# Kernel optimization log

Hardware: AMD Instinct MI355X
Metric: run time of the kernel (lower is better)

## Reference

```python
import jax, jax.numpy as jnp
import numpy as np

N_NODES = 8192
N_EDGES = 262144  # avg degree 32
F_IN = 128
F_OUT = 128


def setup_inputs() -> dict:
    key = jax.random.key(0)
    k1, k2, k3, k4 = jax.random.split(key, 4)
    x = jax.random.normal(k1, (N_NODES, F_IN), dtype=jnp.float32)
    edge_index = jax.random.randint(k2, (2, N_EDGES), 0, N_NODES, dtype=jnp.int32)
    # xavier_uniform-scale random W; B is a learned param (zeros at init, but
    # use random values so the x@B^T branch is exercised numerically)
    scale = np.float32(1.0 / np.sqrt(F_IN))
    W = jax.random.normal(k3, (F_OUT, F_IN), dtype=jnp.float32) * scale
    B = jax.random.normal(k4, (F_OUT, F_IN), dtype=jnp.float32) * scale
    return {"x": x, "edge_index": edge_index, "W": W, "B": B}


def reference(x, edge_index, W, B):
    num_nodes = x.shape[0]
    src, dst = edge_index[0], edge_index[1]
    # Dense adjacency: A[i, j] = 1 iff edge j -> i (duplicate edges collapse to 1,
    # matching torch's adj[dst, src] = 1.0 assignment semantics)
    A = jnp.zeros((num_nodes, num_nodes), dtype=jnp.float32).at[dst, src].set(1.0)
    # In-degree (counts duplicate edges, matching torch.bincount); degree-0 -> 1
    deg = jax.ops.segment_sum(jnp.ones_like(dst, dtype=jnp.float32), dst,
                              num_segments=num_nodes)
    deg = jnp.where(deg == 0, 1.0, deg)
    # D_inv @ A @ x @ W^T + x @ B^T; D_inv is diagonal -> row-scale by 1/deg
    msg = A @ (x @ W.T)           # [N, F_OUT]
    out = msg / deg[:, None] + x @ B.T
    return out
```

## Files before the change

### kernel.cpp

```cpp
#include <hip/hip_runtime.h>
#include <hip/hip_bf16.h>

constexpr int NN = 8192;
constexpr int NE = 262144;
constexpr int FD = 128;
constexpr int CAP = 64;

constexpr size_t H_OFF     = 0;
constexpr size_t H_BYTES   = (size_t)NN * FD * 2;
constexpr size_t CNT_OFF   = H_OFF + H_BYTES;
constexpr size_t CNT_BYTES = (size_t)NN * 4;
constexpr size_t COL_OFF   = CNT_OFF + CNT_BYTES;
constexpr size_t COL_BYTES = (size_t)NN * CAP * 4;
constexpr size_t UB_OFF    = COL_OFF + COL_BYTES;

constexpr int FILL_BLOCKS = 512;
constexpr int GEMM_BLOCKS = 512;

typedef __attribute__((ext_vector_type(8))) short short8;
typedef __attribute__((ext_vector_type(4))) float f32x4;

__device__ __forceinline__ short f2b(float f) {
  union { __hip_bfloat16 b; short s; } u;
  u.b = __float2bfloat16(f);
  return u.s;
}

__device__ __forceinline__ short8 cvt8(float4 a, float4 b) {
  return short8{f2b(a.x), f2b(a.y), f2b(a.z), f2b(a.w),
                f2b(b.x), f2b(b.y), f2b(b.z), f2b(b.w)};
}

__global__ __launch_bounds__(256) void prep_kernel(
    const float* __restrict__ W, const float* __restrict__ Bm,
    short* __restrict__ ub, unsigned int* __restrict__ cnt) {
  const int t = blockIdx.x * 256 + threadIdx.x;
  const float4 f = (t < 4096) ? ((const float4*)W)[t] : ((const float4*)Bm)[t - 4096];
  ((short4*)ub)[t] = short4{f2b(f.x), f2b(f.y), f2b(f.z), f2b(f.w)};
  if (t < 2048) ((uint4*)cnt)[t] = uint4{0u, 0u, 0u, 0u};
}

__global__ __launch_bounds__(256) void fillgemm_kernel(
    const int* __restrict__ ei, unsigned int* __restrict__ cnt,
    int* __restrict__ col, const float* __restrict__ x,
    const short* __restrict__ ub, __hip_bfloat16* __restrict__ h,
    float* __restrict__ out) {
  const int tid = threadIdx.x;

  if (blockIdx.x < FILL_BLOCKS) {
    const int e = (blockIdx.x * 256 + tid) * 2;
    const int2 s2 = *(const int2*)(ei + e);
    const int2 d2 = *(const int2*)(ei + NE + e);
#pragma unroll
    for (int r = 0; r < 2; ++r) {
      const int src = (&s2.x)[r];
      const int dst = (&d2.x)[r];
      const unsigned int pos = atomicAdd(&cnt[dst], 1u);
      if (pos < CAP) col[(size_t)dst * CAP + pos] = src;
    }
    return;
  }

  const int gid = blockIdx.x - FILL_BLOCKS;
  const int bm = (gid >> 2) * 64;
  const int bn = (gid & 3) * 64;
  const int w = tid >> 6;
  const int lane = tid & 63;
  const int l15 = lane & 15;
  const int l4 = lane >> 4;
  const int row0 = bm + w * 16;

  f32x4 acc[4] = {};

#pragma unroll
  for (int kk = 0; kk < 4; ++kk) {
    const int koff = kk * 32 + l4 * 8;
    const float4* xp = (const float4*)(x + (size_t)(row0 + l15) * FD + koff);
    const short8 a = cvt8(xp[0], xp[1]);
#pragma unroll
    for (int ni = 0; ni < 4; ++ni) {
      const short8 b = *(const short8*)(ub + (size_t)(bn + ni * 16 + l15) * FD + koff);
      acc[ni] = __builtin_amdgcn_mfma_f32_16x16x32_bf16(a, b, acc[ni], 0, 0, 0);
    }
  }

#pragma unroll
  for (int ni = 0; ni < 4; ++ni) {
    const int n = bn + ni * 16 + l15;
#pragma unroll
    for (int r = 0; r < 4; ++r) {
      const int row = row0 + l4 * 4 + r;
      const float v = acc[ni][r];
      if (n < FD) h[(size_t)row * FD + n] = __float2bfloat16(v);
      else        out[(size_t)row * FD + (n - FD)] = v;
    }
  }
}

__global__ __launch_bounds__(256) void gather_kernel(
    const unsigned int* __restrict__ h,
    const int* __restrict__ col, const unsigned int* __restrict__ cnt,
    float* __restrict__ out) {
  __shared__ unsigned int bmp[4][NN / 32];

  const int w    = threadIdx.x >> 6;
  const int lane = threadIdx.x & 63;
  const int node = blockIdx.x * 4 + w;
  const int c  = lane & 15;
  const int eu = lane >> 4;
  const unsigned int n = cnt[node];
  const unsigned int nn = (n < (unsigned)CAP) ? n : (unsigned)CAP;
  const int* cl = col + (size_t)node * CAP;

  const int colv = cl[lane];

  ((uint4*)bmp[w])[lane] = uint4{0u, 0u, 0u, 0u};
  __syncthreads();

  int keep = colv;
  if (lane < (int)nn) {
    const unsigned int mask = 1u << (colv & 31);
    const unsigned int old = atomicOr(&bmp[w][colv >> 5], mask);
    if (old & mask) keep = -1;
  }

  float acc[8];
#pragma unroll
  for (int i = 0; i < 8; ++i) acc[i] = 0.f;

  const size_t hstride = FD / 2;

  unsigned int base = 0;
  for (; base + 8 <= nn; base += 8) {
    const int s0 = __shfl(keep, (int)(base + eu), 64);
    const int s1 = __shfl(keep, (int)(base + 4 + eu), 64);
    uint4 v0 = uint4{0u,0u,0u,0u}, v1 = uint4{0u,0u,0u,0u};
    if (s0 >= 0) v0 = *(const uint4*)(h + (size_t)s0 * hstride + (c << 2));
    if (s1 >= 0) v1 = *(const uint4*)(h + (size_t)s1 * hstride + (c << 2));
    acc[0] += __uint_as_float(v0.x << 16) + __uint_as_float(v1.x << 16);
    acc[1] += __uint_as_float(v0.x & 0xffff0000u) + __uint_as_float(v1.x & 0xffff0000u);
    acc[2] += __uint_as_float(v0.y << 16) + __uint_as_float(v1.y << 16);
    acc[3] += __uint_as_float(v0.y & 0xffff0000u) + __uint_as_float(v1.y & 0xffff0000u);
    acc[4] += __uint_as_float(v0.z << 16) + __uint_as_float(v1.z << 16);
    acc[5] += __uint_as_float(v0.z & 0xffff0000u) + __uint_as_float(v1.z & 0xffff0000u);
    acc[6] += __uint_as_float(v0.w << 16) + __uint_as_float(v1.w << 16);
    acc[7] += __uint_as_float(v0.w & 0xffff0000u) + __uint_as_float(v1.w & 0xffff0000u);
  }
  if (base < nn) {
    const unsigned int e0 = base + eu;
    const unsigned int e1 = base + 4 + eu;
    const int s0 = __shfl(keep, (int)e0, 64);
    const int s1 = __shfl(keep, (int)e1, 64);
    uint4 v0 = uint4{0u,0u,0u,0u}, v1 = uint4{0u,0u,0u,0u};
    if (e0 < nn && s0 >= 0) v0 = *(const uint4*)(h + (size_t)s0 * hstride + (c << 2));
    if (e1 < nn && s1 >= 0) v1 = *(const uint4*)(h + (size_t)s1 * hstride + (c << 2));
    acc[0] += __uint_as_float(v0.x << 16) + __uint_as_float(v1.x << 16);
    acc[1] += __uint_as_float(v0.x & 0xffff0000u) + __uint_as_float(v1.x & 0xffff0000u);
    acc[2] += __uint_as_float(v0.y << 16) + __uint_as_float(v1.y << 16);
    acc[3] += __uint_as_float(v0.y & 0xffff0000u) + __uint_as_float(v1.y & 0xffff0000u);
    acc[4] += __uint_as_float(v0.z << 16) + __uint_as_float(v1.z << 16);
    acc[5] += __uint_as_float(v0.z & 0xffff0000u) + __uint_as_float(v1.z & 0xffff0000u);
    acc[6] += __uint_as_float(v0.w << 16) + __uint_as_float(v1.w << 16);
    acc[7] += __uint_as_float(v0.w & 0xffff0000u) + __uint_as_float(v1.w & 0xffff0000u);
  }

#pragma unroll
  for (int i = 0; i < 8; ++i) {
    acc[i] += __shfl_xor(acc[i], 16, 64);
    acc[i] += __shfl_xor(acc[i], 32, 64);
  }

  if (eu == 0) {
    const float r = 1.0f / (n ? (float)n : 1.0f);
    float* op = out + (size_t)node * FD + c * 8;
    float4 o0 = *(float4*)op;
    float4 o1 = *(float4*)(op + 4);
    o0.x += acc[0] * r; o0.y += acc[1] * r; o0.z += acc[2] * r; o0.w += acc[3] * r;
    o1.x += acc[4] * r; o1.y += acc[5] * r; o1.z += acc[6] * r; o1.w += acc[7] * r;
    *(float4*)op = o0;
    *(float4*)(op + 4) = o1;
  }
}

extern "C" void kernel_launch(void* const* d_in, const int* in_sizes, int n_in,
                              void* d_out, int out_size, void* d_ws, size_t ws_size,
                              hipStream_t stream) {
  const float* x  = (const float*)d_in[0];
  const int* ei   = (const int*)d_in[1];
  const float* W  = (const float*)d_in[2];
  const float* Bm = (const float*)d_in[3];
  float* out = (float*)d_out;

  char* ws = (char*)d_ws;
  __hip_bfloat16* h = (__hip_bfloat16*)(ws + H_OFF);
  unsigned int* cnt = (unsigned int*)(ws + CNT_OFF);
  int* col          = (int*)(ws + COL_OFF);
  short* ub         = (short*)(ws + UB_OFF);

  prep_kernel<<<32, 256, 0, stream>>>(W, Bm, ub, cnt);
  fillgemm_kernel<<<FILL_BLOCKS + GEMM_BLOCKS, 256, 0, stream>>>(
      ei, cnt, col, x, ub, h, out);
  gather_kernel<<<NN / 4, 256, 0, stream>>>((const unsigned int*)h, col, cnt, out);
}
```

Before: 37.39 us.

## Split per-node edge counters into 8 privatized groups to reduce atomic contention

The fill phase now spreads its atomic counters and column slots over 8 groups chosen by block index, so concurrent atomics on the same destination node are spread across separate counters. The gather kernel reads the 8 group counts, compacts the group lists into a shared-memory list of up to 64 entries, then deduplicates and gathers as before. This trades atomic contention for 8x larger counter zeroing, an extra compaction pass with block barriers, and scattered 8-segment column reads per node.

```diff
diff --git a/kernel.cpp b/kernel.cpp
--- a/kernel.cpp
+++ b/kernel.cpp
@@ -4,14 +4,15 @@
 constexpr int NN = 8192;
 constexpr int NE = 262144;
 constexpr int FD = 128;
-constexpr int CAP = 64;
+constexpr int NG = 8;
+constexpr unsigned int CAPG = 32;
 
 constexpr size_t H_OFF     = 0;
 constexpr size_t H_BYTES   = (size_t)NN * FD * 2;
 constexpr size_t CNT_OFF   = H_OFF + H_BYTES;
-constexpr size_t CNT_BYTES = (size_t)NN * 4;
+constexpr size_t CNT_BYTES = (size_t)NG * NN * 4;
 constexpr size_t COL_OFF   = CNT_OFF + CNT_BYTES;
-constexpr size_t COL_BYTES = (size_t)NN * CAP * 4;
+constexpr size_t COL_BYTES = (size_t)NN * NG * CAPG * 4;
 constexpr size_t UB_OFF    = COL_OFF + COL_BYTES;
 
 constexpr int FILL_BLOCKS = 512;
@@ -33,21 +34,25 @@
 
 __global__ __launch_bounds__(256) void prep_kernel(
     const float* __restrict__ W, const float* __restrict__ Bm,
-    short* __restrict__ ub, unsigned int* __restrict__ cnt) {
+    short* __restrict__ ub, unsigned int* __restrict__ cnt8) {
   const int t = blockIdx.x * 256 + threadIdx.x;
-  const float4 f = (t < 4096) ? ((const float4*)W)[t] : ((const float4*)Bm)[t - 4096];
-  ((short4*)ub)[t] = short4{f2b(f.x), f2b(f.y), f2b(f.z), f2b(f.w)};
-  if (t < 2048) ((uint4*)cnt)[t] = uint4{0u, 0u, 0u, 0u};
+  if (t < 8192) {
+    const float4 f = (t < 4096) ? ((const float4*)W)[t]
+                                : ((const float4*)Bm)[t - 4096];
+    ((short4*)ub)[t] = short4{f2b(f.x), f2b(f.y), f2b(f.z), f2b(f.w)};
+  }
+  ((uint4*)cnt8)[t] = uint4{0u, 0u, 0u, 0u};
 }
 
 __global__ __launch_bounds__(256) void fillgemm_kernel(
-    const int* __restrict__ ei, unsigned int* __restrict__ cnt,
+    const int* __restrict__ ei, unsigned int* __restrict__ cnt8,
     int* __restrict__ col, const float* __restrict__ x,
     const short* __restrict__ ub, __hip_bfloat16* __restrict__ h,
     float* __restrict__ out) {
   const int tid = threadIdx.x;
 
   if (blockIdx.x < FILL_BLOCKS) {
+    const int g = blockIdx.x & (NG - 1);
     const int e = (blockIdx.x * 256 + tid) * 2;
     const int2 s2 = *(const int2*)(ei + e);
     const int2 d2 = *(const int2*)(ei + NE + e);
@@ -55,8 +60,8 @@
     for (int r = 0; r < 2; ++r) {
       const int src = (&s2.x)[r];
       const int dst = (&d2.x)[r];
-      const unsigned int pos = atomicAdd(&cnt[dst], 1u);
-      if (pos < CAP) col[(size_t)dst * CAP + pos] = src;
+      const unsigned int pos = atomicAdd(&cnt8[(size_t)g * NN + dst], 1u);
+      if (pos < CAPG) col[((size_t)dst * NG + g) * CAPG + pos] = src;
     }
     return;
   }
@@ -99,30 +104,47 @@
 
 __global__ __launch_bounds__(256) void gather_kernel(
     const unsigned int* __restrict__ h,
-    const int* __restrict__ col, const unsigned int* __restrict__ cnt,
+    const int* __restrict__ col, const unsigned int* __restrict__ cnt8,
     float* __restrict__ out) {
   __shared__ unsigned int bmp[4][NN / 32];
+  __shared__ int list[4][64];
 
   const int w    = threadIdx.x >> 6;
   const int lane = threadIdx.x & 63;
   const int node = blockIdx.x * 4 + w;
   const int c  = lane & 15;
   const int eu = lane >> 4;
-  const unsigned int n = cnt[node];
-  const unsigned int nn = (n < (unsigned)CAP) ? n : (unsigned)CAP;
-  const int* cl = col + (size_t)node * CAP;
-
-  const int colv = cl[lane];
+
+  unsigned int cg = 0;
+  if (lane < NG) cg = cnt8[(size_t)lane * NN + node];
 
   ((uint4*)bmp[w])[lane] = uint4{0u, 0u, 0u, 0u};
+  list[w][lane] = -1;
   __syncthreads();
 
-  int keep = colv;
+  unsigned int n_deg = 0, abase = 0;
+#pragma unroll
+  for (int g = 0; g < NG; ++g) {
+    const unsigned int v = __shfl(cg, g, 64);
+    const unsigned int vc = (v < CAPG) ? v : CAPG;
+    const unsigned int idx = abase + lane;
+    if (lane < (int)vc && idx < 64u)
+      list[w][idx] = col[((size_t)node * NG + g) * CAPG + lane];
+    n_deg += v;
+    abase += vc;
+  }
+  const unsigned int nn = (abase < 64u) ? abase : 64u;
+  __syncthreads();
+
   if (lane < (int)nn) {
-    const unsigned int mask = 1u << (colv & 31);
-    const unsigned int old = atomicOr(&bmp[w][colv >> 5], mask);
-    if (old & mask) keep = -1;
-  }
+    const int s = list[w][lane];
+    if (s >= 0) {
+      const unsigned int mask = 1u << (s & 31);
+      const unsigned int old = atomicOr(&bmp[w][s >> 5], mask);
+      if (old & mask) list[w][lane] = -1;
+    }
+  }
+  __syncthreads();
 
   float acc[8];
 #pragma unroll
@@ -130,10 +152,9 @@
 
   const size_t hstride = FD / 2;
 
-  unsigned int base = 0;
-  for (; base + 8 <= nn; base += 8) {
-    const int s0 = __shfl(keep, (int)(base + eu), 64);
-    const int s1 = __shfl(keep, (int)(base + 4 + eu), 64);
+  for (unsigned int base = 0; base < nn; base += 8) {
+    const int s0 = list[w][base + eu];
+    const int s1 = list[w][base + 4 + eu];
     uint4 v0 = uint4{0u,0u,0u,0u}, v1 = uint4{0u,0u,0u,0u};
     if (s0 >= 0) v0 = *(const uint4*)(h + (size_t)s0 * hstride + (c << 2));
     if (s1 >= 0) v1 = *(const uint4*)(h + (size_t)s1 * hstride + (c << 2));
@@ -146,23 +167,6 @@
     acc[6] += __uint_as_float(v0.w << 16) + __uint_as_float(v1.w << 16);
     acc[7] += __uint_as_float(v0.w & 0xffff0000u) + __uint_as_float(v1.w & 0xffff0000u);
   }
-  if (base < nn) {
-    const unsigned int e0 = base + eu;
-    const unsigned int e1 = base + 4 + eu;
-    const int s0 = __shfl(keep, (int)e0, 64);
-    const int s1 = __shfl(keep, (int)e1, 64);
-    uint4 v0 = uint4{0u,0u,0u,0u}, v1 = uint4{0u,0u,0u,0u};
-    if (e0 < nn && s0 >= 0) v0 = *(const uint4*)(h + (size_t)s0 * hstride + (c << 2));
-    if (e1 < nn && s1 >= 0) v1 = *(const uint4*)(h + (size_t)s1 * hstride + (c << 2));
-    acc[0] += __uint_as_float(v0.x << 16) + __uint_as_float(v1.x << 16);
-    acc[1] += __uint_as_float(v0.x & 0xffff0000u) + __uint_as_float(v1.x & 0xffff0000u);
-    acc[2] += __uint_as_float(v0.y << 16) + __uint_as_float(v1.y << 16);
-    acc[3] += __uint_as_float(v0.y & 0xffff0000u) + __uint_as_float(v1.y & 0xffff0000u);
-    acc[4] += __uint_as_float(v0.z << 16) + __uint_as_float(v1.z << 16);
-    acc[5] += __uint_as_float(v0.z & 0xffff0000u) + __uint_as_float(v1.z & 0xffff0000u);
-    acc[6] += __uint_as_float(v0.w << 16) + __uint_as_float(v1.w << 16);
-    acc[7] += __uint_as_float(v0.w & 0xffff0000u) + __uint_as_float(v1.w & 0xffff0000u);
-  }
 
 #pragma unroll
   for (int i = 0; i < 8; ++i) {
@@ -171,7 +175,7 @@
   }
 
   if (eu == 0) {
-    const float r = 1.0f / (n ? (float)n : 1.0f);
+    const float r = 1.0f / (n_deg ? (float)n_deg : 1.0f);
     float* op = out + (size_t)node * FD + c * 8;
     float4 o0 = *(float4*)op;
     float4 o1 = *(float4*)(op + 4);
@@ -192,13 +196,13 @@
   float* out = (float*)d_out;
 
   char* ws = (char*)d_ws;
-  __hip_bfloat16* h = (__hip_bfloat16*)(ws + H_OFF);
-  unsigned int* cnt = (unsigned int*)(ws + CNT_OFF);
-  int* col          = (int*)(ws + COL_OFF);
-  short* ub         = (short*)(ws + UB_OFF);
-
-  prep_kernel<<<32, 256, 0, stream>>>(W, Bm, ub, cnt);
+  __hip_bfloat16* h  = (__hip_bfloat16*)(ws + H_OFF);
+  unsigned int* cnt8 = (unsigned int*)(ws + CNT_OFF);
+  int* col           = (int*)(ws + COL_OFF);
+  short* ub          = (short*)(ws + UB_OFF);
+
+  prep_kernel<<<64, 256, 0, stream>>>(W, Bm, ub, cnt8);
   fillgemm_kernel<<<FILL_BLOCKS + GEMM_BLOCKS, 256, 0, stream>>>(
-      ei, cnt, col, x, ub, h, out);
-  gather_kernel<<<NN / 4, 256, 0, stream>>>((const unsigned int*)h, col, cnt, out);
-}
+      ei, cnt8, col, x, ub, h, out);
+  gather_kernel<<<NN / 4, 256, 0, stream>>>((const unsigned int*)h, col, cnt8, out);
+}
```

Measured after the change: 39.06 us. 1.04x slower.

## Replace capped per-node column lists with a dense adjacency bitmap

Applied to the files above, without the earlier changes.

Edges are now recorded by atomically OR-ing bits into a dense 8192x8192 bitmap (8 MB) in workspace, instead of appending sources into fixed 64-slot column lists. The gather kernel reads each node's 1 KB bitmap row, popcounts it, prefix-scans across the wave and compacts the neighbour ids into a shared-memory list (up to 96) before the bf16 feature gather. Duplicate edges now collapse in the bitmap itself, which removes the per-block shared-memory dedup and the 64-neighbour truncation. The cost is zeroing and later scanning 8 MB of bitmap on every call, which is much more memory traffic than the old 2 MB column array.

```diff
diff --git a/kernel.cpp b/kernel.cpp
--- a/kernel.cpp
+++ b/kernel.cpp
@@ -4,15 +4,17 @@
 constexpr int NN = 8192;
 constexpr int NE = 262144;
 constexpr int FD = 128;
-constexpr int CAP = 64;
+constexpr int LCAP = 96;
 
 constexpr size_t H_OFF     = 0;
 constexpr size_t H_BYTES   = (size_t)NN * FD * 2;
 constexpr size_t CNT_OFF   = H_OFF + H_BYTES;
 constexpr size_t CNT_BYTES = (size_t)NN * 4;
-constexpr size_t COL_OFF   = CNT_OFF + CNT_BYTES;
-constexpr size_t COL_BYTES = (size_t)NN * CAP * 4;
-constexpr size_t UB_OFF    = COL_OFF + COL_BYTES;
+constexpr size_t BMP_OFF   = CNT_OFF + CNT_BYTES;
+constexpr size_t BMP_BYTES = (size_t)NN * NN / 8;
+constexpr size_t UB_OFF    = BMP_OFF + BMP_BYTES;
+
+constexpr int BMP_W = NN / 32;
 
 constexpr int FILL_BLOCKS = 512;
 constexpr int GEMM_BLOCKS = 512;
@@ -33,16 +35,22 @@
 
 __global__ __launch_bounds__(256) void prep_kernel(
     const float* __restrict__ W, const float* __restrict__ Bm,
-    short* __restrict__ ub, unsigned int* __restrict__ cnt) {
+    short* __restrict__ ub, unsigned int* __restrict__ cnt,
+    unsigned int* __restrict__ bmp) {
   const int t = blockIdx.x * 256 + threadIdx.x;
-  const float4 f = (t < 4096) ? ((const float4*)W)[t] : ((const float4*)Bm)[t - 4096];
-  ((short4*)ub)[t] = short4{f2b(f.x), f2b(f.y), f2b(f.z), f2b(f.w)};
-  if (t < 2048) ((uint4*)cnt)[t] = uint4{0u, 0u, 0u, 0u};
+  ((uint4*)bmp)[t] = uint4{0u, 0u, 0u, 0u};
+  if (blockIdx.x < 8) ((uint4*)cnt)[t] = uint4{0u, 0u, 0u, 0u};
+  if (blockIdx.x >= 8 && blockIdx.x < 40) {
+    const int u = t - 2048;
+    const float4 f = (u < 4096) ? ((const float4*)W)[u]
+                                : ((const float4*)Bm)[u - 4096];
+    ((short4*)ub)[u] = short4{f2b(f.x), f2b(f.y), f2b(f.z), f2b(f.w)};
+  }
 }
 
 __global__ __launch_bounds__(256) void fillgemm_kernel(
     const int* __restrict__ ei, unsigned int* __restrict__ cnt,
-    int* __restrict__ col, const float* __restrict__ x,
+    unsigned int* __restrict__ bmp, const float* __restrict__ x,
     const short* __restrict__ ub, __hip_bfloat16* __restrict__ h,
     float* __restrict__ out) {
   const int tid = threadIdx.x;
@@ -55,8 +63,8 @@
     for (int r = 0; r < 2; ++r) {
       const int src = (&s2.x)[r];
       const int dst = (&d2.x)[r];
-      const unsigned int pos = atomicAdd(&cnt[dst], 1u);
-      if (pos < CAP) col[(size_t)dst * CAP + pos] = src;
+      atomicOr(&bmp[(size_t)dst * BMP_W + (src >> 5)], 1u << (src & 31));
+      atomicAdd(&cnt[dst], 1u);
     }
     return;
   }
@@ -99,30 +107,46 @@
 
 __global__ __launch_bounds__(256) void gather_kernel(
     const unsigned int* __restrict__ h,
-    const int* __restrict__ col, const unsigned int* __restrict__ cnt,
+    const unsigned int* __restrict__ bmp, const unsigned int* __restrict__ cnt,
     float* __restrict__ out) {
-  __shared__ unsigned int bmp[4][NN / 32];
+  __shared__ int list[4][LCAP];
 
   const int w    = threadIdx.x >> 6;
   const int lane = threadIdx.x & 63;
   const int node = blockIdx.x * 4 + w;
   const int c  = lane & 15;
   const int eu = lane >> 4;
-  const unsigned int n = cnt[node];
-  const unsigned int nn = (n < (unsigned)CAP) ? n : (unsigned)CAP;
-  const int* cl = col + (size_t)node * CAP;
-
-  const int colv = cl[lane];
-
-  ((uint4*)bmp[w])[lane] = uint4{0u, 0u, 0u, 0u};
+
+  list[w][lane] = -1;
+  if (lane < LCAP - 64) list[w][64 + lane] = -1;
+
+  const uint4 bm = ((const uint4*)(bmp + (size_t)node * BMP_W))[lane];
+  const int cnt4 = __popc(bm.x) + __popc(bm.y) + __popc(bm.z) + __popc(bm.w);
+
+  int inc = cnt4;
+#pragma unroll
+  for (int off = 1; off < 64; off <<= 1) {
+    const int nbr = __shfl_up(inc, off, 64);
+    if (lane >= off) inc += nbr;
+  }
+  const int total = __shfl(inc, 63, 64);
+  int pos = inc - cnt4;
+
+  const int sbase = lane * 128;
+#pragma unroll
+  for (int j = 0; j < 4; ++j) {
+    unsigned int u = (&bm.x)[j];
+    while (u) {
+      const int b = __ffs(u) - 1;
+      u &= u - 1;
+      if (pos < LCAP) list[w][pos] = sbase + j * 32 + b;
+      ++pos;
+    }
+  }
   __syncthreads();
 
-  int keep = colv;
-  if (lane < (int)nn) {
-    const unsigned int mask = 1u << (colv & 31);
-    const unsigned int old = atomicOr(&bmp[w][colv >> 5], mask);
-    if (old & mask) keep = -1;
-  }
+  const int lcnt = (total < LCAP) ? total : LCAP;
+  const unsigned int deg = cnt[node];
 
   float acc[8];
 #pragma unroll
@@ -130,10 +154,9 @@
 
   const size_t hstride = FD / 2;
 
-  unsigned int base = 0;
-  for (; base + 8 <= nn; base += 8) {
-    const int s0 = __shfl(keep, (int)(base + eu), 64);
-    const int s1 = __shfl(keep, (int)(base + 4 + eu), 64);
+  for (int base = 0; base < lcnt; base += 8) {
+    const int s0 = list[w][base + eu];
+    const int s1 = list[w][base + 4 + eu];
     uint4 v0 = uint4{0u,0u,0u,0u}, v1 = uint4{0u,0u,0u,0u};
     if (s0 >= 0) v0 = *(const uint4*)(h + (size_t)s0 * hstride + (c << 2));
     if (s1 >= 0) v1 = *(const uint4*)(h + (size_t)s1 * hstride + (c << 2));
@@ -146,23 +169,6 @@
     acc[6] += __uint_as_float(v0.w << 16) + __uint_as_float(v1.w << 16);
     acc[7] += __uint_as_float(v0.w & 0xffff0000u) + __uint_as_float(v1.w & 0xffff0000u);
   }
-  if (base < nn) {
-    const unsigned int e0 = base + eu;
-    const unsigned int e1 = base + 4 + eu;
-    const int s0 = __shfl(keep, (int)e0, 64);
-    const int s1 = __shfl(keep, (int)e1, 64);
-    uint4 v0 = uint4{0u,0u,0u,0u}, v1 = uint4{0u,0u,0u,0u};
-    if (e0 < nn && s0 >= 0) v0 = *(const uint4*)(h + (size_t)s0 * hstride + (c << 2));
-    if (e1 < nn && s1 >= 0) v1 = *(const uint4*)(h + (size_t)s1 * hstride + (c << 2));
-    acc[0] += __uint_as_float(v0.x << 16) + __uint_as_float(v1.x << 16);
-    acc[1] += __uint_as_float(v0.x & 0xffff0000u) + __uint_as_float(v1.x & 0xffff0000u);
-    acc[2] += __uint_as_float(v0.y << 16) + __uint_as_float(v1.y << 16);
-    acc[3] += __uint_as_float(v0.y & 0xffff0000u) + __uint_as_float(v1.y & 0xffff0000u);
-    acc[4] += __uint_as_float(v0.z << 16) + __uint_as_float(v1.z << 16);
-    acc[5] += __uint_as_float(v0.z & 0xffff0000u) + __uint_as_float(v1.z & 0xffff0000u);
-    acc[6] += __uint_as_float(v0.w << 16) + __uint_as_float(v1.w << 16);
-    acc[7] += __uint_as_float(v0.w & 0xffff0000u) + __uint_as_float(v1.w & 0xffff0000u);
-  }
 
 #pragma unroll
   for (int i = 0; i < 8; ++i) {
@@ -171,7 +177,7 @@
   }
 
   if (eu == 0) {
-    const float r = 1.0f / (n ? (float)n : 1.0f);
+    const float r = 1.0f / (deg ? (float)deg : 1.0f);
     float* op = out + (size_t)node * FD + c * 8;
     float4 o0 = *(float4*)op;
     float4 o1 = *(float4*)(op + 4);
@@ -194,11 +200,11 @@
   char* ws = (char*)d_ws;
   __hip_bfloat16* h = (__hip_bfloat16*)(ws + H_OFF);
   unsigned int* cnt = (unsigned int*)(ws + CNT_OFF);
-  int* col          = (int*)(ws + COL_OFF);
+  unsigned int* bmp = (unsigned int*)(ws + BMP_OFF);
   short* ub         = (short*)(ws + UB_OFF);
 
-  prep_kernel<<<32, 256, 0, stream>>>(W, Bm, ub, cnt);
+  prep_kernel<<<2048, 256, 0, stream>>>(W, Bm, ub, cnt, bmp);
   fillgemm_kernel<<<FILL_BLOCKS + GEMM_BLOCKS, 256, 0, stream>>>(
-      ei, cnt, col, x, ub, h, out);
-  gather_kernel<<<NN / 4, 256, 0, stream>>>((const unsigned int*)h, col, cnt, out);
-}
+      ei, cnt, bmp, x, ub, h, out);
+  gather_kernel<<<NN / 4, 256, 0, stream>>>((const unsigned int*)h, bmp, cnt, out);
+}
```

New measurement: 48.02 us. 1.28x slower.
